# Optimization experiments

Hardware: AMD Instinct MI355X
Metric: run time of the kernel (lower is better)

Reference implementation:

```python
import jax, jax.numpy as jnp
import numpy as np

N = 50000
E = 800000
F_IN = 2      # num_node_features
H = 2         # heads
C = 64        # embedding_size (per-head out channels)
HID = 128     # hidden_size (message dim)
B = 512       # number of messages
NEG_SLOPE = 0.2


def gatv2_conv(x, src, dst, edge_attr, Wl, bl, Wr, br, We, att, bias):
    # x: [N, F_IN]; src/dst: [E]; edge_attr: [E, 1]
    n = x.shape[0]
    xl = (x @ Wl + bl).reshape(n, H, C)   # source transform (lin_l)
    xr = (x @ Wr + br).reshape(n, H, C)   # target transform (lin_r)
    ea = (edge_attr @ We).reshape(-1, H, C)
    m = xl[src] + xr[dst] + ea                      # [E, H, C]
    e = jnp.where(m > 0, m, NEG_SLOPE * m)          # LeakyReLU
    score = jnp.einsum('ehc,hc->eh', e, att)        # [E, H]
    # scatter-softmax over incoming edges of each target node
    smax = jax.ops.segment_max(score, dst, num_segments=n)
    smax = jnp.where(jnp.isfinite(smax), smax, 0.0)
    ex = jnp.exp(score - smax[dst])
    denom = jax.ops.segment_sum(ex, dst, num_segments=n)
    alpha = ex / (denom[dst] + 1e-16)               # [E, H]
    out = jax.ops.segment_sum(xl[src] * alpha[:, :, None], dst, num_segments=n)
    return out.reshape(n, H * C) + bias


def setup_inputs() -> dict:
    key = jax.random.key(0)
    ks = jax.random.split(key, 20)
    s = 0.1
    inp = {
        'message': jax.random.normal(ks[0], (B, HID), jnp.float32),
        'x': jax.random.normal(ks[1], (N, F_IN), jnp.float32),
        'edge_index': jax.random.randint(ks[2], (2, E), 0, N, jnp.int32),
        'edge_attr': jax.random.normal(ks[3], (E, 1), jnp.float32),
    }
    def conv_params(base):
        return {
            'Wl': jax.random.normal(ks[base], (F_IN, H * C)) * s,
            'bl': jnp.zeros((H * C,), jnp.float32),
            'Wr': jax.random.normal(ks[base + 1], (F_IN, H * C)) * s,
            'br': jnp.zeros((H * C,), jnp.float32),
            'We': jax.random.normal(ks[base + 2], (1, H * C)) * s,
            'att': jax.random.normal(ks[base + 3], (H, C)) * s,
            'bias': jnp.zeros((H * C,), jnp.float32),
        }
    p1 = {k + '1': v for k, v in conv_params(4).items()}
    p2 = {k + '2': v for k, v in conv_params(8).items()}
    inp.update(p1)
    inp.update(p2)
    inp['Wfc'] = jax.random.normal(ks[12], (HID, H * C)) * s
    inp['bfc'] = jnp.zeros((H * C,), jnp.float32)
    return inp


def reference(message, x, edge_index, edge_attr,
              Wl1, bl1, Wr1, br1, We1, att1, bias1,
              Wl2, bl2, Wr2, br2, We2, att2, bias2,
              Wfc, bfc):
    src, dst = edge_index[0], edge_index[1]
    # conv1 output is computed but unused in the original forward (conv2 takes x again)
    h1 = jax.nn.relu(gatv2_conv(x, src, dst, edge_attr, Wl1, bl1, Wr1, br1, We1, att1, bias1))
    h = jax.nn.relu(gatv2_conv(x, src, dst, edge_attr, Wl2, bl2, Wr2, br2, We2, att2, bias2))
    msg = jnp.concatenate([message, message], axis=0)      # [2B, HID]
    msg_emb = msg @ Wfc + bfc                              # [2B, H*C]
    dot = h @ msg_emb.T                                    # [N, 2B]
    return jax.nn.softmax(dot, axis=0)
```

## Files before the change

### kernel.cpp

```cpp
#include <hip/hip_runtime.h>
#include <hip/hip_bf16.h>

#define N_NODES 50000
#define N_PAD   50048
#define N_EDGES 800000
#define NB_SCAN 196

typedef __attribute__((ext_vector_type(8))) short short8;
typedef __attribute__((ext_vector_type(4))) float f32x4;
typedef __attribute__((ext_vector_type(16))) float f32x16;

__global__ __launch_bounds__(256) void k_zero(int* __restrict__ buf)
{
  int i = blockIdx.x * 256 + threadIdx.x;
  if (i < N_NODES + 512) buf[i] = 0;
}

__global__ __launch_bounds__(256) void k_hist(
    const int* __restrict__ ei, int* __restrict__ cnt)
{
  int e = blockIdx.x * 256 + threadIdx.x;
  if (e >= N_EDGES) return;
  atomicAdd(&cnt[ei[N_EDGES + e]], 1);
}

__global__ __launch_bounds__(256) void k_scan1(
    const int* __restrict__ cnt, int* __restrict__ offs, int* __restrict__ bsum)
{
  __shared__ int sh[256];
  int b = blockIdx.x, t = threadIdx.x;
  int i = b * 256 + t;
  int v = (i < N_NODES) ? cnt[i] : 0;
  sh[t] = v;
  __syncthreads();
  #pragma unroll
  for (int off = 1; off < 256; off <<= 1) {
    int u = (t >= off) ? sh[t - off] : 0;
    __syncthreads();
    sh[t] += u;
    __syncthreads();
  }
  if (i < N_NODES) offs[i] = sh[t] - v;
  if (t == 255) bsum[b] = sh[255];
}

__global__ __launch_bounds__(256) void k_scan2(int* __restrict__ bsum)
{
  __shared__ int sh[256];
  int t = threadIdx.x;
  int v = (t < NB_SCAN) ? bsum[t] : 0;
  sh[t] = v;
  __syncthreads();
  #pragma unroll
  for (int off = 1; off < 256; off <<= 1) {
    int u = (t >= off) ? sh[t - off] : 0;
    __syncthreads();
    sh[t] += u;
    __syncthreads();
  }
  if (t < NB_SCAN) bsum[t] = sh[t] - v;
}

__global__ __launch_bounds__(256) void k_scan3(
    int* __restrict__ offs, const int* __restrict__ bsum, int* __restrict__ cursor)
{
  int b = blockIdx.x, t = threadIdx.x;
  int i = b * 256 + t;
  if (i < N_NODES) {
    int o = offs[i] + bsum[b];
    offs[i] = o;
    cursor[i] = o;
  }
  if (b == 0 && t == 0) offs[N_NODES] = N_EDGES;
}

__global__ __launch_bounds__(256) void k_scatter(
    const float* __restrict__ x, const int* __restrict__ ei,
    const float* __restrict__ ea,
    const float* __restrict__ Wl, const float* __restrict__ bl,
    const float* __restrict__ Wr, const float* __restrict__ br,
    const float* __restrict__ We, const float* __restrict__ att,
    int* __restrict__ cursor, float4* __restrict__ rec)
{
  int e = blockIdx.x * 256 + threadIdx.x;
  if (e >= N_EDGES) return;
  int s = ei[e], d = ei[N_EDGES + e];
  float x0s = x[2*s], x1s = x[2*s+1];
  float x0d = x[2*d], x1d = x[2*d+1];
  float av = ea[e];

  float s0 = 0.f, s1 = 0.f;
  #pragma unroll 8
  for (int k = 0; k < 64; ++k) {
    float m = bl[k] + br[k];
    m = fmaf(x0s, Wl[k], m);
    m = fmaf(x1s, Wl[128+k], m);
    m = fmaf(x0d, Wr[k], m);
    m = fmaf(x1d, Wr[128+k], m);
    m = fmaf(av, We[k], m);
    float l = m > 0.f ? m : 0.2f * m;
    s0 = fmaf(l, att[k], s0);
  }
  #pragma unroll 8
  for (int k = 64; k < 128; ++k) {
    float m = bl[k] + br[k];
    m = fmaf(x0s, Wl[k], m);
    m = fmaf(x1s, Wl[128+k], m);
    m = fmaf(x0d, Wr[k], m);
    m = fmaf(x1d, Wr[128+k], m);
    m = fmaf(av, We[k], m);
    float l = m > 0.f ? m : 0.2f * m;
    s1 = fmaf(l, att[k], s1);
  }
  int pos = atomicAdd(&cursor[d], 1);
  rec[pos] = make_float4(s0, s1, x0s, x1s);
}

__global__ __launch_bounds__(256) void k_gather(
    const float4* __restrict__ rec, const int* __restrict__ offs,
    float* __restrict__ nodeF)
{
  int n = blockIdx.x * 256 + threadIdx.x;
  if (n >= N_NODES) return;
  int a = offs[n], b = offs[n + 1];
  float D0 = 0.f, A00 = 0.f, A10 = 0.f;
  float D1 = 0.f, A01 = 0.f, A11 = 0.f;
  for (int i = a; i < b; ++i) {
    float4 r = rec[i];
    float e0 = __expf(r.x);
    float e1 = __expf(r.y);
    D0 += e0; A00 += e0 * r.z; A10 += e0 * r.w;
    D1 += e1; A01 += e1 * r.z; A11 += e1 * r.w;
  }
  float* nf = nodeF + (size_t)n * 8;
  nf[0] = D0; nf[1] = A00; nf[2] = A10;
  nf[3] = D1; nf[4] = A01; nf[5] = A11;
}

__global__ __launch_bounds__(128) void k_fc(
    const float* __restrict__ msg, const float* __restrict__ Wfc,
    const float* __restrict__ bfc,
    __hip_bfloat16* __restrict__ me_hi, __hip_bfloat16* __restrict__ me_lo)
{
  int j = blockIdx.x, k = threadIdx.x;
  __shared__ float mrow[128];
  mrow[k] = msg[j*128 + k];
  __syncthreads();
  float acc = bfc[k];
  #pragma unroll 8
  for (int t = 0; t < 128; ++t) acc = fmaf(mrow[t], Wfc[t*128 + k], acc);
  __hip_bfloat16 hi = __float2bfloat16(acc);
  me_hi[j*128 + k] = hi;
  me_lo[j*128 + k] = __float2bfloat16(acc - __bfloat162float(hi));
}

template<int PASS>
__global__ __launch_bounds__(256, 3) void k_mfma(
    const float* __restrict__ nodeF,
    const float* __restrict__ Wl, const float* __restrict__ bl,
    const float* __restrict__ bias,
    const __hip_bfloat16* __restrict__ me_hi, const __hip_bfloat16* __restrict__ me_lo,
    float* __restrict__ colsum, float* __restrict__ dout)
{
  __shared__ short8 Bt[2048];
  __shared__ float colacc[2][512];

  int tid = threadIdx.x;
  int l = tid & 63, w = tid >> 6;
  int rt = w >> 1, ct = w & 1;
  int lrow = l & 31, lhalf = l >> 5;
  int m0 = blockIdx.x * 64;
  int row = m0 + rt * 32 + lrow;

  if (PASS == 0) {
    #pragma unroll
    for (int q = 0; q < 4; ++q) ((float*)colacc)[q * 256 + tid] = 0.f;
  }

  float c0a = 0.f, c0b = 0.f, c0d = 0.f, c1a = 0.f, c1b = 0.f, c1d = 0.f;
  bool live = row < N_NODES;
  if (live) {
    const float* nf = nodeF + (size_t)row * 8;
    float D0 = nf[0], A00 = nf[1], A10 = nf[2];
    float D1 = nf[3], A01 = nf[4], A11 = nf[5];
    float r0 = 1.0f / (D0 + 1e-16f), r1 = 1.0f / (D1 + 1e-16f);
    c0a = A00 * r0; c0b = A10 * r0; c0d = D0 * r0;
    c1a = A01 * r1; c1b = A11 * r1; c1d = D1 * r1;
  }
  short8 a_hi[8], a_lo[8];
  #pragma unroll
  for (int ks = 0; ks < 8; ++ks) {
    int k0 = ks * 16 + lhalf * 8;
    float ca = (ks < 4) ? c0a : c1a;
    float cbv = (ks < 4) ? c0b : c1b;
    float cd = (ks < 4) ? c0d : c1d;
    float wA[8], wB[8], wC[8], wD[8];
    *(float4*)&wA[0] = *(const float4*)(Wl + k0);
    *(float4*)&wA[4] = *(const float4*)(Wl + k0 + 4);
    *(float4*)&wB[0] = *(const float4*)(Wl + 128 + k0);
    *(float4*)&wB[4] = *(const float4*)(Wl + 128 + k0 + 4);
    *(float4*)&wC[0] = *(const float4*)(bl + k0);
    *(float4*)&wC[4] = *(const float4*)(bl + k0 + 4);
    *(float4*)&wD[0] = *(const float4*)(bias + k0);
    *(float4*)&wD[4] = *(const float4*)(bias + k0 + 4);
    short8 hi8, lo8;
    #pragma unroll
    for (int j = 0; j < 8; ++j) {
      float v = ca * wA[j] + cbv * wB[j] + cd * wC[j] + wD[j];
      v = (live && v > 0.f) ? v : 0.f;
      __hip_bfloat16 hb = __float2bfloat16(v);
      float rem = v - __bfloat162float(hb);
      __hip_bfloat16 lb = __float2bfloat16(rem);
      short hs, ls;
      __builtin_memcpy(&hs, &hb, 2);
      __builtin_memcpy(&ls, &lb, 2);
      hi8[j] = hs;
      lo8[j] = ls;
    }
    a_hi[ks] = hi8;
    a_lo[ks] = lo8;
  }

  for (int cb = 0; cb < 8; ++cb) {
    __syncthreads();
    #pragma unroll
    for (int q = 0; q < 4; ++q) {
      int lin = q * 256 + tid;
      int col = lin >> 4, ku = lin & 15;
      int slot = col * 16 + (ku ^ (col & 7));
      size_t gb = ((size_t)(cb * 64 + col) << 7) + ku * 8;
      Bt[slot] = *(const short8*)(me_hi + gb);
      Bt[1024 + slot] = *(const short8*)(me_lo + gb);
    }
    __syncthreads();

    f32x16 acc = {0.f};
    #pragma unroll
    for (int ks = 0; ks < 8; ++ks) {
      int ku = ks * 2 + lhalf;
      int colB = ct * 32 + lrow;
      int slot = colB * 16 + (ku ^ (colB & 7));
      short8 bh = Bt[slot];
      short8 blo = Bt[1024 + slot];
      acc = __builtin_amdgcn_mfma_f32_32x32x16_bf16(a_hi[ks], bh, acc, 0, 0, 0);
      acc = __builtin_amdgcn_mfma_f32_32x32x16_bf16(a_lo[ks], bh, acc, 0, 0, 0);
      acc = __builtin_amdgcn_mfma_f32_32x32x16_bf16(a_hi[ks], blo, acc, 0, 0, 0);
    }

    int col = cb * 64 + ct * 32 + lrow;
    if (PASS == 0) {
      float csum = 0.f;
      #pragma unroll
      for (int i = 0; i < 16; ++i) {
        int grow = m0 + rt * 32 + (i & 3) + 8 * (i >> 2) + 4 * lhalf;
        csum += (grow < N_NODES) ? __expf(acc[i]) : 0.f;
      }
      csum += __shfl_xor(csum, 32);
      if (l < 32) colacc[rt][cb * 64 + ct * 32 + l] += csum;
    } else {
      float rS = 1.0f / colsum[col];
      #pragma unroll
      for (int i = 0; i < 16; ++i) {
        int grow = m0 + rt * 32 + (i & 3) + 8 * (i >> 2) + 4 * lhalf;
        if (grow < N_NODES) {
          float o = __expf(acc[i]) * rS;
          dout[(size_t)grow * 1024 + col] = o;
          dout[(size_t)grow * 1024 + 512 + col] = o;
        }
      }
    }
  }

  if (PASS == 0) {
    __syncthreads();
    atomicAdd(&colsum[tid], colacc[0][tid] + colacc[1][tid]);
    atomicAdd(&colsum[tid + 256], colacc[0][tid + 256] + colacc[1][tid + 256]);
  }
}

extern "C" void kernel_launch(void* const* d_in, const int* in_sizes, int n_in,
                              void* d_out, int out_size, void* d_ws, size_t ws_size,
                              hipStream_t stream)
{
  const float* message = (const float*)d_in[0];
  const float* x       = (const float*)d_in[1];
  const int*   ei      = (const int*)d_in[2];
  const float* ea      = (const float*)d_in[3];
  const float* Wl2   = (const float*)d_in[11];
  const float* bl2   = (const float*)d_in[12];
  const float* Wr2   = (const float*)d_in[13];
  const float* br2   = (const float*)d_in[14];
  const float* We2   = (const float*)d_in[15];
  const float* att2  = (const float*)d_in[16];
  const float* bias2 = (const float*)d_in[17];
  const float* Wfc   = (const float*)d_in[18];
  const float* bfc   = (const float*)d_in[19];

  char* p = (char*)d_ws;
  float4* rec = (float4*)p;                  p += (size_t)N_EDGES * 16;
  float* nodeF = (float*)p;                  p += (size_t)N_NODES * 8 * 4;
  __hip_bfloat16* me_hi = (__hip_bfloat16*)p; p += 512 * 128 * 2;
  __hip_bfloat16* me_lo = (__hip_bfloat16*)p; p += 512 * 128 * 2;
  int* cnt = (int*)p;                        p += (size_t)N_NODES * 4;
  float* colsum = (float*)p;                 p += 512 * 4;
  int* offs = (int*)p;                       p += (size_t)(N_NODES + 1) * 4;
  int* cursor = (int*)p;                     p += (size_t)N_NODES * 4;
  int* bsum = (int*)p;

  float* dout = (float*)d_out;

  k_zero<<<(N_NODES + 512 + 255) / 256, 256, 0, stream>>>(cnt);
  k_hist<<<(N_EDGES + 255) / 256, 256, 0, stream>>>(ei, cnt);
  k_scan1<<<NB_SCAN, 256, 0, stream>>>(cnt, offs, bsum);
  k_scan2<<<1, 256, 0, stream>>>(bsum);
  k_scan3<<<NB_SCAN, 256, 0, stream>>>(offs, bsum, cursor);
  k_scatter<<<(N_EDGES + 255) / 256, 256, 0, stream>>>(
      x, ei, ea, Wl2, bl2, Wr2, br2, We2, att2, cursor, rec);
  k_gather<<<(N_NODES + 255) / 256, 256, 0, stream>>>(rec, offs, nodeF);
  k_fc<<<512, 128, 0, stream>>>(message, Wfc, bfc, me_hi, me_lo);
  k_mfma<0><<<N_PAD / 64, 256, 0, stream>>>(
      nodeF, Wl2, bl2, bias2, me_hi, me_lo, colsum, dout);
  k_mfma<1><<<N_PAD / 64, 256, 0, stream>>>(
      nodeF, Wl2, bl2, bias2, me_hi, me_lo, colsum, dout);
}
```

Before: 255.6 us.

## Fuse whole pipeline into one cooperative persistent kernel with grid syncs

Replaces the chain of ten small kernel launches with a single cooperative kernel of 512 blocks that runs FC, zeroing, histogram, scan, scatter, gather and both MFMA passes, separated by grid-wide syncs. This targets launch gaps and per-kernel tail effects. The MFMA pass-1 output is now staged through LDS and written as coalesced float4 stores instead of scattered scalar stores. The cost is grid-sync overhead, reduced occupancy (2 blocks per CU, 52KB LDS), and grid-stride loops that may load-balance worse than per-element launches. A fallback multi-kernel path remains.

```diff
diff --git a/kernel.cpp b/kernel.cpp
--- a/kernel.cpp
+++ b/kernel.cpp
@@ -1,14 +1,300 @@
 #include <hip/hip_runtime.h>
 #include <hip/hip_bf16.h>
+#include <hip/hip_cooperative_groups.h>
+
+namespace cg = cooperative_groups;
 
 #define N_NODES 50000
 #define N_PAD   50048
 #define N_EDGES 800000
+#define GRID    512
+#define BLK     256
+#define STRIDE  (GRID*BLK)
+#define CHUNK   98
+#define NTILES  782
 #define NB_SCAN 196
 
 typedef __attribute__((ext_vector_type(8))) short short8;
-typedef __attribute__((ext_vector_type(4))) float f32x4;
 typedef __attribute__((ext_vector_type(16))) float f32x16;
+
+struct Params {
+  const float* msg; const float* x; const int* ei; const float* ea;
+  const float* Wl; const float* bl; const float* Wr; const float* br;
+  const float* We; const float* att; const float* bias;
+  const float* Wfc; const float* bfc;
+  float4* rec; float* nodeF;
+  __hip_bfloat16* me_hi; __hip_bfloat16* me_lo;
+  int* cnt; float* colsum; int* offs; int* cursor; int* bsum;
+  float* dout;
+};
+
+template<int PASS>
+__device__ __forceinline__ void mfma_tile(const Params& P, int tile, char* SMEM)
+{
+  short8* Bt = (short8*)SMEM;
+  float* colacc = (float*)(SMEM + 32768);
+  float* xp     = (float*)(SMEM + 32768);
+  float* rcol   = (float*)(SMEM + 50176);
+
+  const int tid = threadIdx.x;
+  const int l = tid & 63, w = tid >> 6;
+  const int rt = w >> 1, ct = w & 1;
+  const int lrow = l & 31, lhalf = l >> 5;
+  const int m0 = tile * 64;
+  const int row = m0 + rt * 32 + lrow;
+
+  float c0a = 0.f, c0b = 0.f, c0d = 0.f, c1a = 0.f, c1b = 0.f, c1d = 0.f;
+  bool live = row < N_NODES;
+  if (live) {
+    const float* nf = P.nodeF + (size_t)row * 8;
+    float D0 = nf[0], A00 = nf[1], A10 = nf[2];
+    float D1 = nf[3], A01 = nf[4], A11 = nf[5];
+    float r0 = 1.0f / (D0 + 1e-16f), r1 = 1.0f / (D1 + 1e-16f);
+    c0a = A00 * r0; c0b = A10 * r0; c0d = D0 * r0;
+    c1a = A01 * r1; c1b = A11 * r1; c1d = D1 * r1;
+  }
+  short8 a_hi[8], a_lo[8];
+  #pragma unroll
+  for (int ks = 0; ks < 8; ++ks) {
+    int k0 = ks * 16 + lhalf * 8;
+    float ca = (ks < 4) ? c0a : c1a;
+    float cbv = (ks < 4) ? c0b : c1b;
+    float cd = (ks < 4) ? c0d : c1d;
+    float wA[8], wB[8], wC[8], wD[8];
+    *(float4*)&wA[0] = *(const float4*)(P.Wl + k0);
+    *(float4*)&wA[4] = *(const float4*)(P.Wl + k0 + 4);
+    *(float4*)&wB[0] = *(const float4*)(P.Wl + 128 + k0);
+    *(float4*)&wB[4] = *(const float4*)(P.Wl + 128 + k0 + 4);
+    *(float4*)&wC[0] = *(const float4*)(P.bl + k0);
+    *(float4*)&wC[4] = *(const float4*)(P.bl + k0 + 4);
+    *(float4*)&wD[0] = *(const float4*)(P.bias + k0);
+    *(float4*)&wD[4] = *(const float4*)(P.bias + k0 + 4);
+    short8 hi8, lo8;
+    #pragma unroll
+    for (int j = 0; j < 8; ++j) {
+      float v = ca * wA[j] + cbv * wB[j] + cd * wC[j] + wD[j];
+      v = (live && v > 0.f) ? v : 0.f;
+      __hip_bfloat16 hb = __float2bfloat16(v);
+      float rem = v - __bfloat162float(hb);
+      __hip_bfloat16 lb = __float2bfloat16(rem);
+      short hs, ls;
+      __builtin_memcpy(&hs, &hb, 2);
+      __builtin_memcpy(&ls, &lb, 2);
+      hi8[j] = hs; lo8[j] = ls;
+    }
+    a_hi[ks] = hi8; a_lo[ks] = lo8;
+  }
+
+  for (int cb = 0; cb < 8; ++cb) {
+    __syncthreads();
+    #pragma unroll
+    for (int q = 0; q < 4; ++q) {
+      int lin = q * 256 + tid;
+      int col = lin >> 4, ku = lin & 15;
+      int slot = col * 16 + (ku ^ (col & 7));
+      size_t gb = ((size_t)(cb * 64 + col) << 7) + ku * 8;
+      Bt[slot] = *(const short8*)(P.me_hi + gb);
+      Bt[1024 + slot] = *(const short8*)(P.me_lo + gb);
+    }
+    __syncthreads();
+
+    f32x16 acc = {0.f};
+    #pragma unroll
+    for (int ks = 0; ks < 8; ++ks) {
+      int ku = ks * 2 + lhalf;
+      int colB = ct * 32 + lrow;
+      int slot = colB * 16 + (ku ^ (colB & 7));
+      short8 bh = Bt[slot];
+      short8 blo = Bt[1024 + slot];
+      acc = __builtin_amdgcn_mfma_f32_32x32x16_bf16(a_hi[ks], bh, acc, 0, 0, 0);
+      acc = __builtin_amdgcn_mfma_f32_32x32x16_bf16(a_lo[ks], bh, acc, 0, 0, 0);
+      acc = __builtin_amdgcn_mfma_f32_32x32x16_bf16(a_hi[ks], blo, acc, 0, 0, 0);
+    }
+
+    if (PASS == 0) {
+      float csum = 0.f;
+      #pragma unroll
+      for (int i = 0; i < 16; ++i) {
+        int grow = m0 + rt * 32 + (i & 3) + 8 * (i >> 2) + 4 * lhalf;
+        csum += (grow < N_NODES) ? __expf(acc[i]) : 0.f;
+      }
+      csum += __shfl_xor(csum, 32);
+      if (l < 32) colacc[rt * 512 + cb * 64 + ct * 32 + l] += csum;
+    } else {
+      #pragma unroll
+      for (int i = 0; i < 16; ++i) {
+        int rl = rt * 32 + (i & 3) + 8 * (i >> 2) + 4 * lhalf;
+        xp[rl * 68 + ct * 32 + lrow] = __expf(acc[i]);
+      }
+      __syncthreads();
+      #pragma unroll
+      for (int q = 0; q < 4; ++q) {
+        int fid = q * 256 + tid;
+        int rl = fid >> 4, c4 = fid & 15;
+        int grow = m0 + rl;
+        float4 v = *(float4*)&xp[rl * 68 + c4 * 4];
+        float4 s = *(const float4*)&rcol[cb * 64 + c4 * 4];
+        v.x *= s.x; v.y *= s.y; v.z *= s.z; v.w *= s.w;
+        if (grow < N_NODES) {
+          *(float4*)&P.dout[(size_t)grow * 1024 + cb * 64 + c4 * 4] = v;
+          *(float4*)&P.dout[(size_t)grow * 1024 + 512 + cb * 64 + c4 * 4] = v;
+        }
+      }
+    }
+  }
+}
+
+__global__ __launch_bounds__(BLK, 2) void k_all(Params P)
+{
+  cg::grid_group gg = cg::this_grid();
+  __shared__ __align__(16) char SMEM[52224];
+  const int b = blockIdx.x, t = threadIdx.x;
+
+  if (b < 256) {
+    float* mrow = (float*)SMEM;
+    int r = 2 * b + (t >> 7);
+    int col = t & 127;
+    mrow[t] = P.msg[r * 128 + col];
+    __syncthreads();
+    int base = (t >> 7) * 128;
+    float acc = P.bfc[col];
+    #pragma unroll 8
+    for (int k = 0; k < 128; ++k) acc = fmaf(mrow[base + k], P.Wfc[k * 128 + col], acc);
+    __hip_bfloat16 hi = __float2bfloat16(acc);
+    P.me_hi[r * 128 + col] = hi;
+    P.me_lo[r * 128 + col] = __float2bfloat16(acc - __bfloat162float(hi));
+  } else if (b < 454) {
+    int i = (b - 256) * 256 + t;
+    if (i < N_NODES + 512) P.cnt[i] = 0;
+  }
+  gg.sync();
+
+  for (int e = b * BLK + t; e < N_EDGES; e += STRIDE)
+    atomicAdd(&P.cnt[P.ei[N_EDGES + e]], 1);
+  gg.sync();
+
+  {
+    int* sh = (int*)SMEM;
+    int base = b * CHUNK;
+    if (t < 128) sh[t] = 0;
+    __syncthreads();
+    int v = 0;
+    if (t < CHUNK && base + t < N_NODES) { v = P.cnt[base + t]; sh[t] = v; }
+    __syncthreads();
+    #pragma unroll
+    for (int off = 1; off < 128; off <<= 1) {
+      int u = (t < 128 && t >= off) ? sh[t - off] : 0;
+      __syncthreads();
+      if (t < 128) sh[t] += u;
+      __syncthreads();
+    }
+    if (t < CHUNK && base + t < N_NODES) P.offs[base + t] = sh[t] - v;
+    if (t == 0) P.bsum[b] = sh[127];
+  }
+  gg.sync();
+
+  {
+    int* eb = (int*)SMEM;
+    int* s3 = eb + 512;
+    int x0 = P.bsum[2 * t], x1 = P.bsum[2 * t + 1];
+    s3[t] = x0 + x1;
+    __syncthreads();
+    #pragma unroll
+    for (int off = 1; off < 256; off <<= 1) {
+      int u = (t >= off) ? s3[t - off] : 0;
+      __syncthreads();
+      s3[t] += u;
+      __syncthreads();
+    }
+    int p = t ? s3[t - 1] : 0;
+    eb[2 * t] = p; eb[2 * t + 1] = p + x0;
+    __syncthreads();
+    int pb = eb[b];
+    int base = b * CHUNK;
+    if (t < CHUNK && base + t < N_NODES) {
+      int o = P.offs[base + t] + pb;
+      P.offs[base + t] = o;
+      P.cursor[base + t] = o;
+    }
+    if (b == 0 && t == 0) P.offs[N_NODES] = N_EDGES;
+  }
+  gg.sync();
+
+  for (int e = b * BLK + t; e < N_EDGES; e += STRIDE) {
+    int s = P.ei[e], d = P.ei[N_EDGES + e];
+    float x0s = P.x[2*s], x1s = P.x[2*s+1];
+    float x0d = P.x[2*d], x1d = P.x[2*d+1];
+    float av = P.ea[e];
+    float s0 = 0.f, s1 = 0.f;
+    #pragma unroll 8
+    for (int k = 0; k < 64; ++k) {
+      float m = P.bl[k] + P.br[k];
+      m = fmaf(x0s, P.Wl[k], m);
+      m = fmaf(x1s, P.Wl[128+k], m);
+      m = fmaf(x0d, P.Wr[k], m);
+      m = fmaf(x1d, P.Wr[128+k], m);
+      m = fmaf(av, P.We[k], m);
+      float lk = m > 0.f ? m : 0.2f * m;
+      s0 = fmaf(lk, P.att[k], s0);
+    }
+    #pragma unroll 8
+    for (int k = 64; k < 128; ++k) {
+      float m = P.bl[k] + P.br[k];
+      m = fmaf(x0s, P.Wl[k], m);
+      m = fmaf(x1s, P.Wl[128+k], m);
+      m = fmaf(x0d, P.Wr[k], m);
+      m = fmaf(x1d, P.Wr[128+k], m);
+      m = fmaf(av, P.We[k], m);
+      float lk = m > 0.f ? m : 0.2f * m;
+      s1 = fmaf(lk, P.att[k], s1);
+    }
+    int pos = atomicAdd(&P.cursor[d], 1);
+    P.rec[pos] = make_float4(s0, s1, x0s, x1s);
+  }
+  gg.sync();
+
+  {
+    int n = b * BLK + t;
+    if (n < N_NODES) {
+      int a = P.offs[n], bb = P.offs[n + 1];
+      float D0 = 0.f, A00 = 0.f, A10 = 0.f;
+      float D1 = 0.f, A01 = 0.f, A11 = 0.f;
+      for (int i = a; i < bb; ++i) {
+        float4 r = P.rec[i];
+        float e0 = __expf(r.x);
+        float e1 = __expf(r.y);
+        D0 += e0; A00 += e0 * r.z; A10 += e0 * r.w;
+        D1 += e1; A01 += e1 * r.z; A11 += e1 * r.w;
+      }
+      float* nf = P.nodeF + (size_t)n * 8;
+      nf[0] = D0; nf[1] = A00; nf[2] = A10;
+      nf[3] = D1; nf[4] = A01; nf[5] = A11;
+    }
+  }
+  gg.sync();
+
+  {
+    float* colacc = (float*)(SMEM + 32768);
+    #pragma unroll
+    for (int q = 0; q < 4; ++q) colacc[q * 256 + t] = 0.f;
+    __syncthreads();
+    for (int tile = b; tile < NTILES; tile += GRID)
+      mfma_tile<0>(P, tile, SMEM);
+    __syncthreads();
+    atomicAdd(&P.colsum[t], colacc[t] + colacc[512 + t]);
+    atomicAdd(&P.colsum[t + 256], colacc[256 + t] + colacc[768 + t]);
+  }
+  gg.sync();
+
+  {
+    float* rcol = (float*)(SMEM + 50176);
+    rcol[t] = 1.0f / P.colsum[t];
+    rcol[t + 256] = 1.0f / P.colsum[t + 256];
+    __syncthreads();
+    for (int tile = b; tile < NTILES; tile += GRID)
+      mfma_tile<1>(P, tile, SMEM);
+  }
+}
 
 __global__ __launch_bounds__(256) void k_zero(int* __restrict__ buf)
 {
@@ -74,207 +360,94 @@
   if (b == 0 && t == 0) offs[N_NODES] = N_EDGES;
 }
 
-__global__ __launch_bounds__(256) void k_scatter(
-    const float* __restrict__ x, const int* __restrict__ ei,
-    const float* __restrict__ ea,
-    const float* __restrict__ Wl, const float* __restrict__ bl,
-    const float* __restrict__ Wr, const float* __restrict__ br,
-    const float* __restrict__ We, const float* __restrict__ att,
-    int* __restrict__ cursor, float4* __restrict__ rec)
+__global__ __launch_bounds__(256) void k_scatter(Params P)
 {
   int e = blockIdx.x * 256 + threadIdx.x;
   if (e >= N_EDGES) return;
-  int s = ei[e], d = ei[N_EDGES + e];
-  float x0s = x[2*s], x1s = x[2*s+1];
-  float x0d = x[2*d], x1d = x[2*d+1];
-  float av = ea[e];
-
+  int s = P.ei[e], d = P.ei[N_EDGES + e];
+  float x0s = P.x[2*s], x1s = P.x[2*s+1];
+  float x0d = P.x[2*d], x1d = P.x[2*d+1];
+  float av = P.ea[e];
   float s0 = 0.f, s1 = 0.f;
   #pragma unroll 8
   for (int k = 0; k < 64; ++k) {
-    float m = bl[k] + br[k];
-    m = fmaf(x0s, Wl[k], m);
-    m = fmaf(x1s, Wl[128+k], m);
-    m = fmaf(x0d, Wr[k], m);
-    m = fmaf(x1d, Wr[128+k], m);
-    m = fmaf(av, We[k], m);
-    float l = m > 0.f ? m : 0.2f * m;
-    s0 = fmaf(l, att[k], s0);
+    float m = P.bl[k] + P.br[k];
+    m = fmaf(x0s, P.Wl[k], m);
+    m = fmaf(x1s, P.Wl[128+k], m);
+    m = fmaf(x0d, P.Wr[k], m);
+    m = fmaf(x1d, P.Wr[128+k], m);
+    m = fmaf(av, P.We[k], m);
+    float lk = m > 0.f ? m : 0.2f * m;
+    s0 = fmaf(lk, P.att[k], s0);
   }
   #pragma unroll 8
   for (int k = 64; k < 128; ++k) {
-    float m = bl[k] + br[k];
-    m = fmaf(x0s, Wl[k], m);
-    m = fmaf(x1s, Wl[128+k], m);
-    m = fmaf(x0d, Wr[k], m);
-    m = fmaf(x1d, Wr[128+k], m);
-    m = fmaf(av, We[k], m);
-    float l = m > 0.f ? m : 0.2f * m;
-    s1 = fmaf(l, att[k], s1);
-  }
-  int pos = atomicAdd(&cursor[d], 1);
-  rec[pos] = make_float4(s0, s1, x0s, x1s);
-}
-
-__global__ __launch_bounds__(256) void k_gather(
-    const float4* __restrict__ rec, const int* __restrict__ offs,
-    float* __restrict__ nodeF)
+    float m = P.bl[k] + P.br[k];
+    m = fmaf(x0s, P.Wl[k], m);
+    m = fmaf(x1s, P.Wl[128+k], m);
+    m = fmaf(x0d, P.Wr[k], m);
+    m = fmaf(x1d, P.Wr[128+k], m);
+    m = fmaf(av, P.We[k], m);
+    float lk = m > 0.f ? m : 0.2f * m;
+    s1 = fmaf(lk, P.att[k], s1);
+  }
+  int pos = atomicAdd(&P.cursor[d], 1);
+  P.rec[pos] = make_float4(s0, s1, x0s, x1s);
+}
+
+__global__ __launch_bounds__(256) void k_gather(Params P)
 {
   int n = blockIdx.x * 256 + threadIdx.x;
   if (n >= N_NODES) return;
-  int a = offs[n], b = offs[n + 1];
+  int a = P.offs[n], b = P.offs[n + 1];
   float D0 = 0.f, A00 = 0.f, A10 = 0.f;
   float D1 = 0.f, A01 = 0.f, A11 = 0.f;
   for (int i = a; i < b; ++i) {
-    float4 r = rec[i];
+    float4 r = P.rec[i];
     float e0 = __expf(r.x);
     float e1 = __expf(r.y);
     D0 += e0; A00 += e0 * r.z; A10 += e0 * r.w;
     D1 += e1; A01 += e1 * r.z; A11 += e1 * r.w;
   }
-  float* nf = nodeF + (size_t)n * 8;
+  float* nf = P.nodeF + (size_t)n * 8;
   nf[0] = D0; nf[1] = A00; nf[2] = A10;
   nf[3] = D1; nf[4] = A01; nf[5] = A11;
 }
 
-__global__ __launch_bounds__(128) void k_fc(
-    const float* __restrict__ msg, const float* __restrict__ Wfc,
-    const float* __restrict__ bfc,
-    __hip_bfloat16* __restrict__ me_hi, __hip_bfloat16* __restrict__ me_lo)
+__global__ __launch_bounds__(128) void k_fc(Params P)
 {
   int j = blockIdx.x, k = threadIdx.x;
   __shared__ float mrow[128];
-  mrow[k] = msg[j*128 + k];
+  mrow[k] = P.msg[j*128 + k];
   __syncthreads();
-  float acc = bfc[k];
+  float acc = P.bfc[k];
   #pragma unroll 8
-  for (int t = 0; t < 128; ++t) acc = fmaf(mrow[t], Wfc[t*128 + k], acc);
+  for (int t = 0; t < 128; ++t) acc = fmaf(mrow[t], P.Wfc[t*128 + k], acc);
   __hip_bfloat16 hi = __float2bfloat16(acc);
-  me_hi[j*128 + k] = hi;
-  me_lo[j*128 + k] = __float2bfloat16(acc - __bfloat162float(hi));
+  P.me_hi[j*128 + k] = hi;
+  P.me_lo[j*128 + k] = __float2bfloat16(acc - __bfloat162float(hi));
 }
 
 template<int PASS>
-__global__ __launch_bounds__(256, 3) void k_mfma(
-    const float* __restrict__ nodeF,
-    const float* __restrict__ Wl, const float* __restrict__ bl,
-    const float* __restrict__ bias,
-    const __hip_bfloat16* __restrict__ me_hi, const __hip_bfloat16* __restrict__ me_lo,
-    float* __restrict__ colsum, float* __restrict__ dout)
-{
-  __shared__ short8 Bt[2048];
-  __shared__ float colacc[2][512];
-
+__global__ __launch_bounds__(256, 2) void k_mfma(Params P)
+{
+  __shared__ __align__(16) char SMEM[52224];
   int tid = threadIdx.x;
-  int l = tid & 63, w = tid >> 6;
-  int rt = w >> 1, ct = w & 1;
-  int lrow = l & 31, lhalf = l >> 5;
-  int m0 = blockIdx.x * 64;
-  int row = m0 + rt * 32 + lrow;
-
   if (PASS == 0) {
-    #pragma unroll
-    for (int q = 0; q < 4; ++q) ((float*)colacc)[q * 256 + tid] = 0.f;
-  }
-
-  float c0a = 0.f, c0b = 0.f, c0d = 0.f, c1a = 0.f, c1b = 0.f, c1d = 0.f;
-  bool live = row < N_NODES;
-  if (live) {
-    const float* nf = nodeF + (size_t)row * 8;
-    float D0 = nf[0], A00 = nf[1], A10 = nf[2];
-    float D1 = nf[3], A01 = nf[4], A11 = nf[5];
-    float r0 = 1.0f / (D0 + 1e-16f), r1 = 1.0f / (D1 + 1e-16f);
-    c0a = A00 * r0; c0b = A10 * r0; c0d = D0 * r0;
-    c1a = A01 * r1; c1b = A11 * r1; c1d = D1 * r1;
-  }
-  short8 a_hi[8], a_lo[8];
-  #pragma unroll
-  for (int ks = 0; ks < 8; ++ks) {
-    int k0 = ks * 16 + lhalf * 8;
-    float ca = (ks < 4) ? c0a : c1a;
-    float cbv = (ks < 4) ? c0b : c1b;
-    float cd = (ks < 4) ? c0d : c1d;
-    float wA[8], wB[8], wC[8], wD[8];
-    *(float4*)&wA[0] = *(const float4*)(Wl + k0);
-    *(float4*)&wA[4] = *(const float4*)(Wl + k0 + 4);
-    *(float4*)&wB[0] = *(const float4*)(Wl + 128 + k0);
-    *(float4*)&wB[4] = *(const float4*)(Wl + 128 + k0 + 4);
-    *(float4*)&wC[0] = *(const float4*)(bl + k0);
-    *(float4*)&wC[4] = *(const float4*)(bl + k0 + 4);
-    *(float4*)&wD[0] = *(const float4*)(bias + k0);
-    *(float4*)&wD[4] = *(const float4*)(bias + k0 + 4);
-    short8 hi8, lo8;
-    #pragma unroll
-    for (int j = 0; j < 8; ++j) {
-      float v = ca * wA[j] + cbv * wB[j] + cd * wC[j] + wD[j];
-      v = (live && v > 0.f) ? v : 0.f;
-      __hip_bfloat16 hb = __float2bfloat16(v);
-      float rem = v - __bfloat162float(hb);
-      __hip_bfloat16 lb = __float2bfloat16(rem);
-      short hs, ls;
-      __builtin_memcpy(&hs, &hb, 2);
-      __builtin_memcpy(&ls, &lb, 2);
-      hi8[j] = hs;
-      lo8[j] = ls;
-    }
-    a_hi[ks] = hi8;
-    a_lo[ks] = lo8;
-  }
-
-  for (int cb = 0; cb < 8; ++cb) {
-    __syncthreads();
-    #pragma unroll
-    for (int q = 0; q < 4; ++q) {
-      int lin = q * 256 + tid;
-      int col = lin >> 4, ku = lin & 15;
-      int slot = col * 16 + (ku ^ (col & 7));
-      size_t gb = ((size_t)(cb * 64 + col) << 7) + ku * 8;
-      Bt[slot] = *(const short8*)(me_hi + gb);
-      Bt[1024 + slot] = *(const short8*)(me_lo + gb);
-    }
-    __syncthreads();
-
-    f32x16 acc = {0.f};
-    #pragma unroll
-    for (int ks = 0; ks < 8; ++ks) {
-      int ku = ks * 2 + lhalf;
-      int colB = ct * 32 + lrow;
-      int slot = colB * 16 + (ku ^ (colB & 7));
-      short8 bh = Bt[slot];
-      short8 blo = Bt[1024 + slot];
-      acc = __builtin_amdgcn_mfma_f32_32x32x16_bf16(a_hi[ks], bh, acc, 0, 0, 0);
-      acc = __builtin_amdgcn_mfma_f32_32x32x16_bf16(a_lo[ks], bh, acc, 0, 0, 0);
-      acc = __builtin_amdgcn_mfma_f32_32x32x16_bf16(a_hi[ks], blo, acc, 0, 0, 0);
-    }
-
-    int col = cb * 64 + ct * 32 + lrow;
-    if (PASS == 0) {
-      float csum = 0.f;
-      #pragma unroll
-      for (int i = 0; i < 16; ++i) {
-        int grow = m0 + rt * 32 + (i & 3) + 8 * (i >> 2) + 4 * lhalf;
-        csum += (grow < N_NODES) ? __expf(acc[i]) : 0.f;
-      }
-      csum += __shfl_xor(csum, 32);
-      if (l < 32) colacc[rt][cb * 64 + ct * 32 + l] += csum;
-    } else {
-      float rS = 1.0f / colsum[col];
-      #pragma unroll
-      for (int i = 0; i < 16; ++i) {
-        int grow = m0 + rt * 32 + (i & 3) + 8 * (i >> 2) + 4 * lhalf;
-        if (grow < N_NODES) {
-          float o = __expf(acc[i]) * rS;
-          dout[(size_t)grow * 1024 + col] = o;
-          dout[(size_t)grow * 1024 + 512 + col] = o;
-        }
-      }
-    }
-  }
-
-  if (PASS == 0) {
-    __syncthreads();
-    atomicAdd(&colsum[tid], colacc[0][tid] + colacc[1][tid]);
-    atomicAdd(&colsum[tid + 256], colacc[0][tid + 256] + colacc[1][tid + 256]);
+    float* colacc = (float*)(SMEM + 32768);
+    #pragma unroll
+    for (int q = 0; q < 4; ++q) colacc[q * 256 + tid] = 0.f;
+    __syncthreads();
+    mfma_tile<0>(P, blockIdx.x, SMEM);
+    __syncthreads();
+    atomicAdd(&P.colsum[tid], colacc[tid] + colacc[512 + tid]);
+    atomicAdd(&P.colsum[tid + 256], colacc[256 + tid] + colacc[768 + tid]);
+  } else {
+    float* rcol = (float*)(SMEM + 50176);
+    rcol[tid] = 1.0f / P.colsum[tid];
+    rcol[tid + 256] = 1.0f / P.colsum[tid + 256];
+    __syncthreads();
+    mfma_tile<1>(P, blockIdx.x, SMEM);
   }
 }
 
@@ -282,44 +455,50 @@
                               void* d_out, int out_size, void* d_ws, size_t ws_size,
                               hipStream_t stream)
 {
-  const float* message = (const float*)d_in[0];
-  const float* x       = (const float*)d_in[1];
-  const int*   ei      = (const int*)d_in[2];
-  const float* ea      = (const float*)d_in[3];
-  const float* Wl2   = (const float*)d_in[11];
-  const float* bl2   = (const float*)d_in[12];
-  const float* Wr2   = (const float*)d_in[13];
-  const float* br2   = (const float*)d_in[14];
-  const float* We2   = (const float*)d_in[15];
-  const float* att2  = (const float*)d_in[16];
-  const float* bias2 = (const float*)d_in[17];
-  const float* Wfc   = (const float*)d_in[18];
-  const float* bfc   = (const float*)d_in[19];
+  Params P;
+  P.msg = (const float*)d_in[0];
+  P.x   = (const float*)d_in[1];
+  P.ei  = (const int*)d_in[2];
+  P.ea  = (const float*)d_in[3];
+  P.Wl   = (const float*)d_in[11];
+  P.bl   = (const float*)d_in[12];
+  P.Wr   = (const float*)d_in[13];
+  P.br   = (const float*)d_in[14];
+  P.We   = (const float*)d_in[15];
+  P.att  = (const float*)d_in[16];
+  P.bias = (const float*)d_in[17];
+  P.Wfc  = (const float*)d_in[18];
+  P.bfc  = (const float*)d_in[19];
 
   char* p = (char*)d_ws;
-  float4* rec = (float4*)p;                  p += (size_t)N_EDGES * 16;
-  float* nodeF = (float*)p;                  p += (size_t)N_NODES * 8 * 4;
-  __hip_bfloat16* me_hi = (__hip_bfloat16*)p; p += 512 * 128 * 2;
-  __hip_bfloat16* me_lo = (__hip_bfloat16*)p; p += 512 * 128 * 2;
-  int* cnt = (int*)p;                        p += (size_t)N_NODES * 4;
-  float* colsum = (float*)p;                 p += 512 * 4;
-  int* offs = (int*)p;                       p += (size_t)(N_NODES + 1) * 4;
-  int* cursor = (int*)p;                     p += (size_t)N_NODES * 4;
-  int* bsum = (int*)p;
-
-  float* dout = (float*)d_out;
-
-  k_zero<<<(N_NODES + 512 + 255) / 256, 256, 0, stream>>>(cnt);
-  k_hist<<<(N_EDGES + 255) / 256, 256, 0, stream>>>(ei, cnt);
-  k_scan1<<<NB_SCAN, 256, 0, stream>>>(cnt, offs, bsum);
-  k_scan2<<<1, 256, 0, stream>>>(bsum);
-  k_scan3<<<NB_SCAN, 256, 0, stream>>>(offs, bsum, cursor);
-  k_scatter<<<(N_EDGES + 255) / 256, 256, 0, stream>>>(
-      x, ei, ea, Wl2, bl2, Wr2, br2, We2, att2, cursor, rec);
-  k_gather<<<(N_NODES + 255) / 256, 256, 0, stream>>>(rec, offs, nodeF);
-  k_fc<<<512, 128, 0, stream>>>(message, Wfc, bfc, me_hi, me_lo);
-  k_mfma<0><<<N_PAD / 64, 256, 0, stream>>>(
-      nodeF, Wl2, bl2, bias2, me_hi, me_lo, colsum, dout);
-  k_mfma<1><<<N_PAD / 64, 256, 0, stream>>>(
-      nodeF, Wl2, bl2, bias2, me_hi, me_lo, colsum, dout);
-}
+  P.rec = (float4*)p;                    p += (size_t)N_EDGES * 16;
+  P.nodeF = (float*)p;                   p += (size_t)N_NODES * 8 * 4;
+  P.me_hi = (__hip_bfloat16*)p;          p += 512 * 128 * 2;
+  P.me_lo = (__hip_bfloat16*)p;          p += 512 * 128 * 2;
+  P.cnt = (int*)p;                       p += (size_t)N_NODES * 4;
+  P.colsum = (float*)p;                  p += 512 * 4;
+  P.offs = (int*)p;                      p += (size_t)(N_NODES + 1) * 4;
+  P.cursor = (int*)p;                    p += (size_t)N_NODES * 4;
+  P.bsum = (int*)p;                      p += GRID * 4;
+  P.dout = (float*)d_out;
+
+  int maxBlk = 0;
+  hipError_t qerr = hipOccupancyMaxActiveBlocksPerMultiprocessor(&maxBlk, k_all, BLK, 0);
+  if (qerr == hipSuccess && maxBlk >= 2) {
+    void* args[] = { &P };
+    hipError_t lerr = hipLaunchCooperativeKernel((void*)k_all, dim3(GRID), dim3(BLK),
+                                                 args, 0, stream);
+    if (lerr == hipSuccess) return;
+  }
+
+  k_zero<<<(N_NODES + 512 + 255) / 256, 256, 0, stream>>>(P.cnt);
+  k_hist<<<(N_EDGES + 255) / 256, 256, 0, stream>>>(P.ei, P.cnt);
+  k_scan1<<<NB_SCAN, 256, 0, stream>>>(P.cnt, P.offs, P.bsum);
+  k_scan2<<<1, 256, 0, stream>>>(P.bsum);
+  k_scan3<<<NB_SCAN, 256, 0, stream>>>(P.offs, P.bsum, P.cursor);
+  k_scatter<<<(N_EDGES + 255) / 256, 256, 0, stream>>>(P);
+  k_gather<<<(N_NODES + 255) / 256, 256, 0, stream>>>(P);
+  k_fc<<<512, 128, 0, stream>>>(P);
+  k_mfma<0><<<NTILES, 256, 0, stream>>>(P);
+  k_mfma<1><<<NTILES, 256, 0, stream>>>(P);
+}
```

Result: faster. 216.0 us (-15.5%).
